# Kernel optimization log

Hardware: AMD Instinct MI355X
Metric: run time of the kernel (lower is better)

Reference implementation:

```python
import jax, jax.numpy as jnp
import numpy as np

EPS = 1e-3  # BatchNorm eps from module

def _bn(x, g, b, m, v):
    # torch BatchNorm1d (eval): (x - mean) / sqrt(var + eps) * weight + bias
    return (x - m) * (g / jnp.sqrt(v + EPS)) + b

def setup_inputs() -> dict:
    key = jax.random.key(0)
    ks = jax.random.split(key, 16)
    N, Cin, Cout, S = 1_000_000, 16, 64, 20_000
    inputs = jax.random.normal(ks[0], (N, Cin), dtype=jnp.float32)
    unq_inv = jax.random.randint(ks[1], (N,), 0, S, dtype=jnp.int32)

    def bn_params(k, c):
        k1, k2, k3, k4 = jax.random.split(k, 4)
        return (1.0 + 0.01 * jax.random.normal(k1, (c,), jnp.float32),
                0.01 * jax.random.normal(k2, (c,), jnp.float32),
                0.01 * jax.random.normal(k3, (c,), jnp.float32),
                jax.random.uniform(k4, (c,), jnp.float32, 0.5, 1.5))

    W1 = 0.1 * jax.random.normal(ks[2], (Cin, Cout), jnp.float32)
    g1, b1, m1, v1 = bn_params(ks[3], Cout)
    W2a = 0.1 * jax.random.normal(ks[4], (Cin, 2 * Cout), jnp.float32)
    g2a, b2a, m2a, v2a = bn_params(ks[5], 2 * Cout)
    W2b = 0.1 * jax.random.normal(ks[6], (2 * Cout, Cout), jnp.float32)
    g2b, b2b, m2b, v2b = bn_params(ks[7], Cout)

    return dict(inputs=inputs, unq_inv=unq_inv, num_segments=S,
                W1=W1, g1=g1, b1=b1, m1=m1, v1=v1,
                W2a=W2a, g2a=g2a, b2a=b2a, m2a=m2a, v2a=v2a,
                W2b=W2b, g2b=b2b * 0 + g2b, b2b=b2b, m2b=m2b, v2b=v2b)

def reference(inputs, unq_inv, num_segments,
              W1, g1, b1, m1, v1,
              W2a, g2a, b2a, m2a, v2a,
              W2b, g2b, b2b, m2b, v2b):
    # branch 1: Linear -> BN -> ReLU
    x = jax.nn.relu(_bn(inputs @ W1, g1, b1, m1, v1))            # [N, C]
    # branch 2: Linear -> BN -> ReLU -> Linear -> BN -> ReLU
    h = jax.nn.relu(_bn(inputs @ W2a, g2a, b2a, m2a, v2a))       # [N, 2C]
    x2 = jax.nn.relu(_bn(h @ W2b, g2b, b2b, m2b, v2b))           # [N, C]

    # segment reductions over group ids
    x_max = jax.ops.segment_max(x, unq_inv, num_segments=num_segments)  # [S, C]
    x_max = jnp.maximum(x_max, 0.0)  # empty segments -> 0 (x >= 0 post-ReLU)
    group_sum = jax.ops.segment_sum(x, unq_inv, num_segments=num_segments)  # [S, C]
    max_pool = jnp.max(x2, axis=0)                                # [C], global pool
    max_pool = jnp.broadcast_to(max_pool[None, :], x_max.shape)   # [S, C]

    feat = jnp.concatenate((group_sum, x_max, max_pool), axis=1)  # [S, 3C]
    # channel shuffle with groups=3
    S_, C3 = feat.shape
    feat = feat.reshape(S_, 3, C3 // 3).transpose(0, 2, 1).reshape(S_, C3)
    return feat
```

## Files before the change

### kernel.cpp

```cpp
#include <hip/hip_runtime.h>

#define EPS 1e-3f

#define OFF_T2B    7168
#define OFF_MPP    7232
#define OFF_MPF    11328
#define OFF_CNT    11392
#define OFF_OFFS   31408
#define OFF_CUR    51424
#define OFF_INPS   71424

typedef short short8 __attribute__((ext_vector_type(8)));
typedef float f32x4 __attribute__((ext_vector_type(4)));

union U4 { unsigned u[4]; short8 s8; uint4 u4; };

__device__ inline unsigned short f2bf(float f) {
    unsigned u = __float_as_uint(f);
    return (unsigned short)((u + 0x7FFFu + ((u >> 16) & 1u)) >> 16);
}

__global__ __launch_bounds__(256) void init_k(
    const float* __restrict__ W1,
    const float* __restrict__ g1, const float* __restrict__ b1,
    const float* __restrict__ m1, const float* __restrict__ v1,
    const float* __restrict__ W2a,
    const float* __restrict__ g2a, const float* __restrict__ b2a,
    const float* __restrict__ m2a, const float* __restrict__ v2a,
    const float* __restrict__ W2b,
    const float* __restrict__ g2b, const float* __restrict__ b2b,
    const float* __restrict__ m2b, const float* __restrict__ v2b,
    unsigned short* __restrict__ wsu, float* __restrict__ wsf,
    const int* __restrict__ unq, int* __restrict__ cnt, int N)
{
    const int t = threadIdx.x;
    if (blockIdx.x == 0) {
        for (int i = t; i < 2048; i += 256) {
            int mt = i >> 9, lane = (i >> 3) & 63, j = i & 7;
            int c = lane & 15, g = lane >> 4;
            int k = g * 8 + j, ch = mt * 16 + c;
            float s = g1[ch] * rsqrtf(v1[ch] + EPS);
            float val = (k < 16) ? W1[k * 64 + ch] * s
                      : (k == 16 ? b1[ch] - m1[ch] * s : 0.f);
            wsu[i] = f2bf(val);
        }
        for (int i = t; i < 4096; i += 256) {
            int mt = i >> 9, lane = (i >> 3) & 63, j = i & 7;
            int c = lane & 15, g = lane >> 4;
            int k = g * 8 + j, ch = mt * 16 + c;
            float s = g2a[ch] * rsqrtf(v2a[ch] + EPS);
            float val = (k < 16) ? W2a[k * 128 + ch] * s
                      : (k == 16 ? b2a[ch] - m2a[ch] * s : 0.f);
            wsu[2048 + i] = f2bf(val);
        }
        for (int i = t; i < 8192; i += 256) {
            int f = i >> 9, lane = (i >> 3) & 63, j = i & 7;
            int mt = f >> 2, ks = f & 3;
            int c = lane & 15, g = lane >> 4;
            int k = ks * 32 + g * 8 + j, ch = mt * 16 + c;
            float s = g2b[ch] * rsqrtf(v2b[ch] + EPS);
            wsu[6144 + i] = f2bf(W2b[k * 64 + ch] * s);
        }
        if (t < 64) {
            float s = g2b[t] * rsqrtf(v2b[t] + EPS);
            wsf[OFF_T2B + t] = b2b[t] - m2b[t] * s;
        }
    } else {
        const int i = (blockIdx.x - 1) * 256 + t;
        if (i < N) atomicAdd(&cnt[unq[i]], 1);
    }
}

__global__ __launch_bounds__(1024) void scan_k(
    const int* __restrict__ cnt, int* __restrict__ offs,
    int* __restrict__ cur, int S)
{
    __shared__ int tot[1024];
    const int t = threadIdx.x;
    const int E = (S + 1023) >> 10;
    const int i0 = t * E;
    int run = 0;
    for (int j = 0; j < E; ++j) {
        const int i = i0 + j;
        run += (i < S) ? cnt[i] : 0;
    }
    tot[t] = run;
    __syncthreads();
    for (int d = 1; d < 1024; d <<= 1) {
        int x = (t >= d) ? tot[t - d] : 0;
        __syncthreads();
        tot[t] += x;
        __syncthreads();
    }
    int base = (t == 0) ? 0 : tot[t - 1];
    for (int j = 0; j < E; ++j) {
        const int i = i0 + j;
        if (i < S) {
            offs[i] = base;
            cur[i]  = base;
            base += cnt[i];
        }
    }
    if (t == 1023) offs[S] = tot[1023];
}

__global__ __launch_bounds__(256, 3) void scatbr2_k(
    const float* __restrict__ inputs,
    const int*   __restrict__ unq,
    int*         __restrict__ cur,
    uint4*       __restrict__ inpS,
    const uint4* __restrict__ wsw,
    const float* __restrict__ wsf,
    float* __restrict__ mpp,
    int N)
{
    __shared__ __align__(16) char scrs[4][2][4096];
    __shared__ float mpb[64];

    const int tid  = threadIdx.x;
    const int wv   = tid >> 6;
    const int lane = tid & 63;
    const int c = lane & 15;
    const int g = lane >> 4;

    if (tid < 64) mpb[tid] = 0.f;
    __syncthreads();

    short8 w2a[8], w2b[16];
    #pragma unroll
    for (int mt = 0; mt < 8; ++mt) {
        U4 t; t.u4 = wsw[256 + mt * 64 + lane]; w2a[mt] = t.s8;
    }
    #pragma unroll
    for (int f = 0; f < 16; ++f) {
        U4 t; t.u4 = wsw[768 + f * 64 + lane]; w2b[f] = t.s8;
    }

    const long wave_pt0 = (long)blockIdx.x * 256 + (long)wv * 64;
    const long nrem_w = (long)N - wave_pt0;

    const long ip = wave_pt0 + lane;
    const bool lane_ok = (ip < (long)N) && (nrem_w > 0);
    int pos = 0;
    if (lane_ok) pos = atomicAdd(&cur[unq[ip]], 1);

    const f32x4 zero4 = {0.f, 0.f, 0.f, 0.f};
    float mp[16];
    #pragma unroll
    for (int j = 0; j < 16; ++j) mp[j] = -3.0e38f;

    #pragma unroll
    for (int ti = 0; ti < 4; ++ti) {
        if ((long)ti * 16 >= nrem_w) break;
        const bool act = (long)(ti * 16 + c) < nrem_w;
        char* scr = scrs[wv][ti & 1];

        U4 bf;
        if (g < 2) {
            const long row = act ? (wave_pt0 + ti * 16 + c) : (long)(N - 1);
            const float4* p = reinterpret_cast<const float4*>(inputs + row * 16 + g * 8);
            float4 f0 = p[0], f1 = p[1];
            asm("v_cvt_pk_bf16_f32 %0, %1, %2" : "=v"(bf.u[0]) : "v"(f0.x), "v"(f0.y));
            asm("v_cvt_pk_bf16_f32 %0, %1, %2" : "=v"(bf.u[1]) : "v"(f0.z), "v"(f0.w));
            asm("v_cvt_pk_bf16_f32 %0, %1, %2" : "=v"(bf.u[2]) : "v"(f1.x), "v"(f1.y));
            asm("v_cvt_pk_bf16_f32 %0, %1, %2" : "=v"(bf.u[3]) : "v"(f1.z), "v"(f1.w));
            if (!act) { bf.u[0] = 0u; bf.u[1] = 0u; bf.u[2] = 0u; bf.u[3] = 0u; }
        } else {
            bf.u[0] = (g == 2 && act) ? 0x00003F80u : 0u;
            bf.u[1] = 0u; bf.u[2] = 0u; bf.u[3] = 0u;
        }

        const int posc = __shfl(pos, ti * 16 + c, 64);
        if (g < 2 && act)
            inpS[(size_t)posc * 2 + g] = bf.u4;

        __builtin_amdgcn_wave_barrier();
        #pragma unroll
        for (int mt = 0; mt < 8; ++mt) {
            f32x4 hT = __builtin_amdgcn_mfma_f32_16x16x32_bf16(w2a[mt], bf.s8, zero4, 0, 0, 0);
            float h0 = fmaxf(hT[0], 0.f), h1 = fmaxf(hT[1], 0.f);
            float h2 = fmaxf(hT[2], 0.f), h3 = fmaxf(hT[3], 0.f);
            unsigned lo, hi;
            asm("v_cvt_pk_bf16_f32 %0, %1, %2" : "=v"(lo) : "v"(h0), "v"(h1));
            asm("v_cvt_pk_bf16_f32 %0, %1, %2" : "=v"(hi) : "v"(h2), "v"(h3));
            const int gw = 2 * (mt & 1) + (g >> 1);
            *reinterpret_cast<uint2*>(
                &scr[(mt >> 1) * 1024 + (gw * 16 + c) * 16 + (g & 1) * 8])
                = make_uint2(lo, hi);
        }
        __builtin_amdgcn_wave_barrier();

        f32x4 y2t[4];
        #pragma unroll
        for (int mt = 0; mt < 4; ++mt) y2t[mt] = zero4;
        #pragma unroll
        for (int ks = 0; ks < 4; ++ks) {
            short8 hb = *reinterpret_cast<const short8*>(&scr[ks * 1024 + lane * 16]);
            #pragma unroll
            for (int mt = 0; mt < 4; ++mt)
                y2t[mt] = __builtin_amdgcn_mfma_f32_16x16x32_bf16(w2b[mt * 4 + ks], hb, y2t[mt], 0, 0, 0);
        }
        #pragma unroll
        for (int mt = 0; mt < 4; ++mt) {
            #pragma unroll
            for (int r = 0; r < 4; ++r)
                mp[mt * 4 + r] = act ? fmaxf(mp[mt * 4 + r], y2t[mt][r]) : mp[mt * 4 + r];
        }
        __builtin_amdgcn_wave_barrier();
    }

    #pragma unroll
    for (int j = 0; j < 16; ++j) {
        float x = mp[j];
        x = fmaxf(x, __shfl_xor(x, 1, 64));
        x = fmaxf(x, __shfl_xor(x, 2, 64));
        x = fmaxf(x, __shfl_xor(x, 4, 64));
        x = fmaxf(x, __shfl_xor(x, 8, 64));
        mp[j] = x;
    }
    if (c == 0) {
        #pragma unroll
        for (int mt = 0; mt < 4; ++mt)
            #pragma unroll
            for (int r = 0; r < 4; ++r) {
                const int ch = mt * 16 + g * 4 + r;
                const float v = fmaxf(mp[mt * 4 + r] + wsf[OFF_T2B + ch], 0.f);
                atomicMax(reinterpret_cast<int*>(&mpb[ch]), __float_as_int(v));
            }
    }
    __syncthreads();
    if (tid < 64)
        atomicMax(reinterpret_cast<int*>(mpp + (blockIdx.x & 63) * 64 + tid),
                  __float_as_int(mpb[tid]));
}

__global__ __launch_bounds__(64) void fin_k(
    const float* __restrict__ mpp, float* __restrict__ mpf)
{
    const int t = threadIdx.x;
    float m = 0.f;
    #pragma unroll
    for (int s = 0; s < 64; ++s)
        m = fmaxf(m, mpp[s * 64 + t]);
    mpf[t] = m;
}

__global__ __launch_bounds__(256, 6) void seg1_k(
    const uint4* __restrict__ inpS,
    const int*   __restrict__ offs,
    const uint4* __restrict__ wsw,
    const float* __restrict__ mpf,
    float* __restrict__ out,
    int S)
{
    __shared__ float scr3[4][192];

    const int tid  = threadIdx.x;
    const int wv   = tid >> 6;
    const int lane = tid & 63;
    const int seg  = blockIdx.x * 4 + wv;
    if (seg >= S) return;

    const int c = lane & 15;
    const int g = lane >> 4;

    short8 w1[4];
    #pragma unroll
    for (int mt = 0; mt < 4; ++mt) {
        U4 t; t.u4 = wsw[mt * 64 + lane]; w1[mt] = t.s8;
    }
    const float mpl = mpf[lane];

    const int su    = __builtin_amdgcn_readfirstlane(seg);
    const int start = offs[su];
    const int end   = offs[su + 1];

    const f32x4 zero4 = {0.f, 0.f, 0.f, 0.f};
    f32x4 as[4], am[4];
    #pragma unroll
    for (int mt = 0; mt < 4; ++mt) { as[mt] = zero4; am[mt] = zero4; }

    for (int base = start; base < end; base += 64) {
        const int nrem = end - base;
        #pragma unroll
        for (int ti = 0; ti < 4; ++ti) {
            if (ti * 16 >= nrem) break;
            const bool act = (ti * 16 + c) < nrem;

            U4 bf;
            if (g < 2) {
                const int row = min(base + ti * 16 + c, end - 1);
                uint4 q = inpS[(size_t)row * 2 + g];
                bf.u[0] = act ? q.x : 0u;
                bf.u[1] = act ? q.y : 0u;
                bf.u[2] = act ? q.z : 0u;
                bf.u[3] = act ? q.w : 0u;
            } else {
                bf.u[0] = (g == 2 && act) ? 0x00003F80u : 0u;
                bf.u[1] = 0u; bf.u[2] = 0u; bf.u[3] = 0u;
            }
            #pragma unroll
            for (int mt = 0; mt < 4; ++mt) {
                f32x4 y1t = __builtin_amdgcn_mfma_f32_16x16x32_bf16(w1[mt], bf.s8, zero4, 0, 0, 0);
                #pragma unroll
                for (int r = 0; r < 4; ++r) {
                    float v = fmaxf(y1t[r], 0.f);
                    as[mt][r] += v;
                    am[mt][r]  = fmaxf(am[mt][r], v);
                }
            }
        }
    }

    #pragma unroll
    for (int mt = 0; mt < 4; ++mt) {
        #pragma unroll
        for (int r = 0; r < 4; ++r) {
            float xs = as[mt][r], xm = am[mt][r];
            xs += __shfl_xor(xs, 1, 64);  xm = fmaxf(xm, __shfl_xor(xm, 1, 64));
            xs += __shfl_xor(xs, 2, 64);  xm = fmaxf(xm, __shfl_xor(xm, 2, 64));
            xs += __shfl_xor(xs, 4, 64);  xm = fmaxf(xm, __shfl_xor(xm, 4, 64));
            xs += __shfl_xor(xs, 8, 64);  xm = fmaxf(xm, __shfl_xor(xm, 8, 64));
            as[mt][r] = xs; am[mt][r] = xm;
        }
    }

    float* sr = scr3[wv];
    if (c == 0) {
        #pragma unroll
        for (int mt = 0; mt < 4; ++mt)
            #pragma unroll
            for (int r = 0; r < 4; ++r) {
                const int ch = mt * 16 + g * 4 + r;
                sr[ch * 3 + 0] = as[mt][r];
                sr[ch * 3 + 1] = am[mt][r];
            }
    }
    sr[lane * 3 + 2] = mpl;
    __builtin_amdgcn_wave_barrier();
    asm volatile("s_waitcnt lgkmcnt(0)" ::: "memory");
    __builtin_amdgcn_sched_barrier(0);

    float* o = out + (size_t)seg * 192;
    #pragma unroll
    for (int p = 0; p < 3; ++p)
        o[p * 64 + lane] = sr[p * 64 + lane];
}

extern "C" void kernel_launch(void* const* d_in, const int* in_sizes, int n_in,
                              void* d_out, int out_size, void* d_ws, size_t ws_size,
                              hipStream_t stream)
{
    const float* inputs = (const float*)d_in[0];
    const int*   unq    = (const int*)d_in[1];
    const float* W1  = (const float*)d_in[3];
    const float* g1  = (const float*)d_in[4];
    const float* b1  = (const float*)d_in[5];
    const float* m1  = (const float*)d_in[6];
    const float* v1  = (const float*)d_in[7];
    const float* W2a = (const float*)d_in[8];
    const float* g2a = (const float*)d_in[9];
    const float* b2a = (const float*)d_in[10];
    const float* m2a = (const float*)d_in[11];
    const float* v2a = (const float*)d_in[12];
    const float* W2b = (const float*)d_in[13];
    const float* g2b = (const float*)d_in[14];
    const float* b2b = (const float*)d_in[15];
    const float* m2b = (const float*)d_in[16];
    const float* v2b = (const float*)d_in[17];

    float* wsf = (float*)d_ws;
    float* out = (float*)d_out;
    const int N = in_sizes[0] / 16;
    const int S = out_size / 192;

    float* mpp  = wsf + OFF_MPP;
    float* mpf  = wsf + OFF_MPF;
    int*   cnt  = (int*)(wsf + OFF_CNT);
    int*   offs = (int*)(wsf + OFF_OFFS);
    int*   cur  = (int*)(wsf + OFF_CUR);
    uint4* inpS = (uint4*)(wsf + OFF_INPS);

    hipMemsetAsync(mpp, 0, (size_t)(OFF_CNT + 20016 - OFF_MPP) * sizeof(float), stream);

    init_k<<<1 + (N + 255) / 256, 256, 0, stream>>>(
        W1, g1, b1, m1, v1, W2a, g2a, b2a, m2a, v2a, W2b, g2b, b2b, m2b, v2b,
        (unsigned short*)d_ws, wsf, unq, cnt, N);

    scan_k<<<1, 1024, 0, stream>>>(cnt, offs, cur, S);

    scatbr2_k<<<(N + 255) / 256, 256, 0, stream>>>(inputs, unq, cur, inpS,
                                                   (const uint4*)d_ws, wsf, mpp, N);

    fin_k<<<1, 64, 0, stream>>>(mpp, mpf);

    seg1_k<<<(S + 3) / 4, 256, 0, stream>>>(inpS, offs, (const uint4*)d_ws,
                                            mpf, out, S);
}
```

Measured before the change: 208.9 us.

## Split scatter from branch-2 kernel, move histogram into persistent branch-2 grid

Moves the segment-count atomics out of init_k into a persistent grid-stride branch-2 kernel, and splits the bf16 scatter into its own one-row-per-thread kernel that runs after the scan. This lets the branch-2 MLP and max-pool run before the prefix scan. The cost is an extra kernel launch and a second full read of the inputs. seg1_k also becomes a persistent 1024-block grid-stride loop with its occupancy hint lowered from 6 to 4, and asm barriers pin the branch-2 weights in registers.

```diff
diff --git a/kernel.cpp b/kernel.cpp
--- a/kernel.cpp
+++ b/kernel.cpp
@@ -30,44 +30,38 @@
     const float* __restrict__ W2b,
     const float* __restrict__ g2b, const float* __restrict__ b2b,
     const float* __restrict__ m2b, const float* __restrict__ v2b,
-    unsigned short* __restrict__ wsu, float* __restrict__ wsf,
-    const int* __restrict__ unq, int* __restrict__ cnt, int N)
+    unsigned short* __restrict__ wsu, float* __restrict__ wsf)
 {
     const int t = threadIdx.x;
-    if (blockIdx.x == 0) {
-        for (int i = t; i < 2048; i += 256) {
-            int mt = i >> 9, lane = (i >> 3) & 63, j = i & 7;
-            int c = lane & 15, g = lane >> 4;
-            int k = g * 8 + j, ch = mt * 16 + c;
-            float s = g1[ch] * rsqrtf(v1[ch] + EPS);
-            float val = (k < 16) ? W1[k * 64 + ch] * s
-                      : (k == 16 ? b1[ch] - m1[ch] * s : 0.f);
-            wsu[i] = f2bf(val);
-        }
-        for (int i = t; i < 4096; i += 256) {
-            int mt = i >> 9, lane = (i >> 3) & 63, j = i & 7;
-            int c = lane & 15, g = lane >> 4;
-            int k = g * 8 + j, ch = mt * 16 + c;
-            float s = g2a[ch] * rsqrtf(v2a[ch] + EPS);
-            float val = (k < 16) ? W2a[k * 128 + ch] * s
-                      : (k == 16 ? b2a[ch] - m2a[ch] * s : 0.f);
-            wsu[2048 + i] = f2bf(val);
-        }
-        for (int i = t; i < 8192; i += 256) {
-            int f = i >> 9, lane = (i >> 3) & 63, j = i & 7;
-            int mt = f >> 2, ks = f & 3;
-            int c = lane & 15, g = lane >> 4;
-            int k = ks * 32 + g * 8 + j, ch = mt * 16 + c;
-            float s = g2b[ch] * rsqrtf(v2b[ch] + EPS);
-            wsu[6144 + i] = f2bf(W2b[k * 64 + ch] * s);
-        }
-        if (t < 64) {
-            float s = g2b[t] * rsqrtf(v2b[t] + EPS);
-            wsf[OFF_T2B + t] = b2b[t] - m2b[t] * s;
-        }
-    } else {
-        const int i = (blockIdx.x - 1) * 256 + t;
-        if (i < N) atomicAdd(&cnt[unq[i]], 1);
+    for (int i = t; i < 2048; i += 256) {
+        int mt = i >> 9, lane = (i >> 3) & 63, j = i & 7;
+        int c = lane & 15, g = lane >> 4;
+        int k = g * 8 + j, ch = mt * 16 + c;
+        float s = g1[ch] * rsqrtf(v1[ch] + EPS);
+        float val = (k < 16) ? W1[k * 64 + ch] * s
+                  : (k == 16 ? b1[ch] - m1[ch] * s : 0.f);
+        wsu[i] = f2bf(val);
+    }
+    for (int i = t; i < 4096; i += 256) {
+        int mt = i >> 9, lane = (i >> 3) & 63, j = i & 7;
+        int c = lane & 15, g = lane >> 4;
+        int k = g * 8 + j, ch = mt * 16 + c;
+        float s = g2a[ch] * rsqrtf(v2a[ch] + EPS);
+        float val = (k < 16) ? W2a[k * 128 + ch] * s
+                  : (k == 16 ? b2a[ch] - m2a[ch] * s : 0.f);
+        wsu[2048 + i] = f2bf(val);
+    }
+    for (int i = t; i < 8192; i += 256) {
+        int f = i >> 9, lane = (i >> 3) & 63, j = i & 7;
+        int mt = f >> 2, ks = f & 3;
+        int c = lane & 15, g = lane >> 4;
+        int k = ks * 32 + g * 8 + j, ch = mt * 16 + c;
+        float s = g2b[ch] * rsqrtf(v2b[ch] + EPS);
+        wsu[6144 + i] = f2bf(W2b[k * 64 + ch] * s);
+    }
+    if (t < 64) {
+        float s = g2b[t] * rsqrtf(v2b[t] + EPS);
+        wsf[OFF_T2B + t] = b2b[t] - m2b[t] * s;
     }
 }
 
@@ -104,11 +98,10 @@
     if (t == 1023) offs[S] = tot[1023];
 }
 
-__global__ __launch_bounds__(256, 3) void scatbr2_k(
+__global__ __launch_bounds__(256, 3) void br2_k(
     const float* __restrict__ inputs,
     const int*   __restrict__ unq,
-    int*         __restrict__ cur,
-    uint4*       __restrict__ inpS,
+    int*         __restrict__ cnt,
     const uint4* __restrict__ wsw,
     const float* __restrict__ wsf,
     float* __restrict__ mpp,
@@ -128,85 +121,85 @@
 
     short8 w2a[8], w2b[16];
     #pragma unroll
-    for (int mt = 0; mt < 8; ++mt) {
-        U4 t; t.u4 = wsw[256 + mt * 64 + lane]; w2a[mt] = t.s8;
+    for (int s = 0; s < 8; ++s) {
+        U4 t; t.u4 = wsw[256 + s * 64 + lane]; w2a[s] = t.s8;
     }
     #pragma unroll
     for (int f = 0; f < 16; ++f) {
         U4 t; t.u4 = wsw[768 + f * 64 + lane]; w2b[f] = t.s8;
     }
-
-    const long wave_pt0 = (long)blockIdx.x * 256 + (long)wv * 64;
-    const long nrem_w = (long)N - wave_pt0;
-
-    const long ip = wave_pt0 + lane;
-    const bool lane_ok = (ip < (long)N) && (nrem_w > 0);
-    int pos = 0;
-    if (lane_ok) pos = atomicAdd(&cur[unq[ip]], 1);
+    #pragma unroll
+    for (int s = 0; s < 8; ++s) asm volatile("" : "+v"(w2a[s]));
+    #pragma unroll
+    for (int f = 0; f < 16; ++f) asm volatile("" : "+v"(w2b[f]));
 
     const f32x4 zero4 = {0.f, 0.f, 0.f, 0.f};
     float mp[16];
     #pragma unroll
     for (int j = 0; j < 16; ++j) mp[j] = -3.0e38f;
 
-    #pragma unroll
-    for (int ti = 0; ti < 4; ++ti) {
-        if ((long)ti * 16 >= nrem_w) break;
-        const bool act = (long)(ti * 16 + c) < nrem_w;
-        char* scr = scrs[wv][ti & 1];
-
-        U4 bf;
-        if (g < 2) {
-            const long row = act ? (wave_pt0 + ti * 16 + c) : (long)(N - 1);
-            const float4* p = reinterpret_cast<const float4*>(inputs + row * 16 + g * 8);
-            float4 f0 = p[0], f1 = p[1];
-            asm("v_cvt_pk_bf16_f32 %0, %1, %2" : "=v"(bf.u[0]) : "v"(f0.x), "v"(f0.y));
-            asm("v_cvt_pk_bf16_f32 %0, %1, %2" : "=v"(bf.u[1]) : "v"(f0.z), "v"(f0.w));
-            asm("v_cvt_pk_bf16_f32 %0, %1, %2" : "=v"(bf.u[2]) : "v"(f1.x), "v"(f1.y));
-            asm("v_cvt_pk_bf16_f32 %0, %1, %2" : "=v"(bf.u[3]) : "v"(f1.z), "v"(f1.w));
-            if (!act) { bf.u[0] = 0u; bf.u[1] = 0u; bf.u[2] = 0u; bf.u[3] = 0u; }
-        } else {
-            bf.u[0] = (g == 2 && act) ? 0x00003F80u : 0u;
-            bf.u[1] = 0u; bf.u[2] = 0u; bf.u[3] = 0u;
+    const long stride = (long)gridDim.x * 256;
+    for (long base = (long)blockIdx.x * 256 + (long)wv * 64; base < N; base += stride) {
+        const long nrem_w = (long)N - base;
+
+        if (lane < nrem_w) atomicAdd(&cnt[unq[base + lane]], 1);
+
+        #pragma unroll
+        for (int ti = 0; ti < 4; ++ti) {
+            if ((long)ti * 16 >= nrem_w) break;
+            const bool act = (long)(ti * 16 + c) < nrem_w;
+            char* scr = scrs[wv][ti & 1];
+
+            U4 bf;
+            if (g < 2) {
+                const long row = act ? (base + ti * 16 + c) : (long)(N - 1);
+                const float4* p = reinterpret_cast<const float4*>(inputs + row * 16 + g * 8);
+                float4 f0 = p[0], f1 = p[1];
+                asm("v_cvt_pk_bf16_f32 %0, %1, %2" : "=v"(bf.u[0]) : "v"(f0.x), "v"(f0.y));
+                asm("v_cvt_pk_bf16_f32 %0, %1, %2" : "=v"(bf.u[1]) : "v"(f0.z), "v"(f0.w));
+                asm("v_cvt_pk_bf16_f32 %0, %1, %2" : "=v"(bf.u[2]) : "v"(f1.x), "v"(f1.y));
+                asm("v_cvt_pk_bf16_f32 %0, %1, %2" : "=v"(bf.u[3]) : "v"(f1.z), "v"(f1.w));
+                if (!act) { bf.u[0] = 0u; bf.u[1] = 0u; bf.u[2] = 0u; bf.u[3] = 0u; }
+            } else {
+                bf.u[0] = (g == 2 && act) ? 0x00003F80u : 0u;
+                bf.u[1] = 0u; bf.u[2] = 0u; bf.u[3] = 0u;
+            }
+
+            __builtin_amdgcn_wave_barrier();
+            #pragma unroll
+            for (int mt = 0; mt < 8; ++mt) {
+                f32x4 hT = __builtin_amdgcn_mfma_f32_16x16x32_bf16(w2a[mt], bf.s8, zero4, 0, 0, 0);
+                float h0 = fmaxf(hT[0], 0.f), h1 = fmaxf(hT[1], 0.f);
+                float h2 = fmaxf(hT[2], 0.f), h3 = fmaxf(hT[3], 0.f);
+                unsigned lo, hi;
+                asm("v_cvt_pk_bf16_f32 %0, %1, %2" : "=v"(lo) : "v"(h0), "v"(h1));
+                asm("v_cvt_pk_bf16_f32 %0, %1, %2" : "=v"(hi) : "v"(h2), "v"(h3));
+                const int gw = 2 * (mt & 1) + (g >> 1);
+                *reinterpret_cast<uint2*>(
+                    &scr[(mt >> 1) * 1024 + (gw * 16 + c) * 16 + (g & 1) * 8])
+                    = make_uint2(lo, hi);
+            }
+            __builtin_amdgcn_wave_barrier();
+
+            f32x4 y2t[4];
+            #pragma unroll
+            for (int mt = 0; mt < 4; ++mt) y2t[mt] = zero4;
+            #pragma unroll
+            for (int ks = 0; ks < 4; ++ks) {
+                short8 hb = *reinterpret_cast<const short8*>(&scr[ks * 1024 + lane * 16]);
+                #pragma unroll
+                for (int mt = 0; mt < 4; ++mt)
+                    y2t[mt] = __builtin_amdgcn_mfma_f32_16x16x32_bf16(w2b[mt * 4 + ks], hb, y2t[mt], 0, 0, 0);
+            }
+            #pragma unroll
+            for (int mt = 0; mt < 4; ++mt) {
+                #pragma unroll
+                for (int r = 0; r < 4; ++r)
+                    mp[mt * 4 + r] = act ? fmaxf(mp[mt * 4 + r], y2t[mt][r])
+                                         : mp[mt * 4 + r];
+            }
+            __builtin_amdgcn_wave_barrier();
         }
-
-        const int posc = __shfl(pos, ti * 16 + c, 64);
-        if (g < 2 && act)
-            inpS[(size_t)posc * 2 + g] = bf.u4;
-
-        __builtin_amdgcn_wave_barrier();
-        #pragma unroll
-        for (int mt = 0; mt < 8; ++mt) {
-            f32x4 hT = __builtin_amdgcn_mfma_f32_16x16x32_bf16(w2a[mt], bf.s8, zero4, 0, 0, 0);
-            float h0 = fmaxf(hT[0], 0.f), h1 = fmaxf(hT[1], 0.f);
-            float h2 = fmaxf(hT[2], 0.f), h3 = fmaxf(hT[3], 0.f);
-            unsigned lo, hi;
-            asm("v_cvt_pk_bf16_f32 %0, %1, %2" : "=v"(lo) : "v"(h0), "v"(h1));
-            asm("v_cvt_pk_bf16_f32 %0, %1, %2" : "=v"(hi) : "v"(h2), "v"(h3));
-            const int gw = 2 * (mt & 1) + (g >> 1);
-            *reinterpret_cast<uint2*>(
-                &scr[(mt >> 1) * 1024 + (gw * 16 + c) * 16 + (g & 1) * 8])
-                = make_uint2(lo, hi);
-        }
-        __builtin_amdgcn_wave_barrier();
-
-        f32x4 y2t[4];
-        #pragma unroll
-        for (int mt = 0; mt < 4; ++mt) y2t[mt] = zero4;
-        #pragma unroll
-        for (int ks = 0; ks < 4; ++ks) {
-            short8 hb = *reinterpret_cast<const short8*>(&scr[ks * 1024 + lane * 16]);
-            #pragma unroll
-            for (int mt = 0; mt < 4; ++mt)
-                y2t[mt] = __builtin_amdgcn_mfma_f32_16x16x32_bf16(w2b[mt * 4 + ks], hb, y2t[mt], 0, 0, 0);
-        }
-        #pragma unroll
-        for (int mt = 0; mt < 4; ++mt) {
-            #pragma unroll
-            for (int r = 0; r < 4; ++r)
-                mp[mt * 4 + r] = act ? fmaxf(mp[mt * 4 + r], y2t[mt][r]) : mp[mt * 4 + r];
-        }
-        __builtin_amdgcn_wave_barrier();
     }
 
     #pragma unroll
@@ -234,6 +227,34 @@
                   __float_as_int(mpb[tid]));
 }
 
+__global__ __launch_bounds__(256) void scat_k(
+    const float* __restrict__ inputs,
+    const int*   __restrict__ unq,
+    int*         __restrict__ cur,
+    uint4*       __restrict__ inpS,
+    int N)
+{
+    const int i = blockIdx.x * 256 + threadIdx.x;
+    if (i >= N) return;
+    const int seg = unq[i];
+    const int pos = atomicAdd(&cur[seg], 1);
+
+    const float4* p = reinterpret_cast<const float4*>(inputs + (size_t)i * 16);
+    float4 a0 = p[0], a1 = p[1], a2 = p[2], a3 = p[3];
+    unsigned pk[8];
+    asm("v_cvt_pk_bf16_f32 %0, %1, %2" : "=v"(pk[0]) : "v"(a0.x), "v"(a0.y));
+    asm("v_cvt_pk_bf16_f32 %0, %1, %2" : "=v"(pk[1]) : "v"(a0.z), "v"(a0.w));
+    asm("v_cvt_pk_bf16_f32 %0, %1, %2" : "=v"(pk[2]) : "v"(a1.x), "v"(a1.y));
+    asm("v_cvt_pk_bf16_f32 %0, %1, %2" : "=v"(pk[3]) : "v"(a1.z), "v"(a1.w));
+    asm("v_cvt_pk_bf16_f32 %0, %1, %2" : "=v"(pk[4]) : "v"(a2.x), "v"(a2.y));
+    asm("v_cvt_pk_bf16_f32 %0, %1, %2" : "=v"(pk[5]) : "v"(a2.z), "v"(a2.w));
+    asm("v_cvt_pk_bf16_f32 %0, %1, %2" : "=v"(pk[6]) : "v"(a3.x), "v"(a3.y));
+    asm("v_cvt_pk_bf16_f32 %0, %1, %2" : "=v"(pk[7]) : "v"(a3.z), "v"(a3.w));
+
+    inpS[(size_t)pos * 2]     = make_uint4(pk[0], pk[1], pk[2], pk[3]);
+    inpS[(size_t)pos * 2 + 1] = make_uint4(pk[4], pk[5], pk[6], pk[7]);
+}
+
 __global__ __launch_bounds__(64) void fin_k(
     const float* __restrict__ mpp, float* __restrict__ mpf)
 {
@@ -245,7 +266,7 @@
     mpf[t] = m;
 }
 
-__global__ __launch_bounds__(256, 6) void seg1_k(
+__global__ __launch_bounds__(256, 4) void seg1_k(
     const uint4* __restrict__ inpS,
     const int*   __restrict__ offs,
     const uint4* __restrict__ wsw,
@@ -258,9 +279,6 @@
     const int tid  = threadIdx.x;
     const int wv   = tid >> 6;
     const int lane = tid & 63;
-    const int seg  = blockIdx.x * 4 + wv;
-    if (seg >= S) return;
-
     const int c = lane & 15;
     const int g = lane >> 4;
 
@@ -270,81 +288,85 @@
         U4 t; t.u4 = wsw[mt * 64 + lane]; w1[mt] = t.s8;
     }
     const float mpl = mpf[lane];
-
-    const int su    = __builtin_amdgcn_readfirstlane(seg);
-    const int start = offs[su];
-    const int end   = offs[su + 1];
-
+    float* sr = scr3[wv];
     const f32x4 zero4 = {0.f, 0.f, 0.f, 0.f};
-    f32x4 as[4], am[4];
-    #pragma unroll
-    for (int mt = 0; mt < 4; ++mt) { as[mt] = zero4; am[mt] = zero4; }
-
-    for (int base = start; base < end; base += 64) {
-        const int nrem = end - base;
+
+    const int nw = gridDim.x * 4;
+    for (int seg = blockIdx.x * 4 + wv; seg < S; seg += nw) {
+        const int su    = __builtin_amdgcn_readfirstlane(seg);
+        const int start = offs[su];
+        const int end   = offs[su + 1];
+
+        f32x4 as[4], am[4];
         #pragma unroll
-        for (int ti = 0; ti < 4; ++ti) {
-            if (ti * 16 >= nrem) break;
-            const bool act = (ti * 16 + c) < nrem;
-
-            U4 bf;
-            if (g < 2) {
-                const int row = min(base + ti * 16 + c, end - 1);
-                uint4 q = inpS[(size_t)row * 2 + g];
-                bf.u[0] = act ? q.x : 0u;
-                bf.u[1] = act ? q.y : 0u;
-                bf.u[2] = act ? q.z : 0u;
-                bf.u[3] = act ? q.w : 0u;
-            } else {
-                bf.u[0] = (g == 2 && act) ? 0x00003F80u : 0u;
-                bf.u[1] = 0u; bf.u[2] = 0u; bf.u[3] = 0u;
-            }
-            #pragma unroll
-            for (int mt = 0; mt < 4; ++mt) {
-                f32x4 y1t = __builtin_amdgcn_mfma_f32_16x16x32_bf16(w1[mt], bf.s8, zero4, 0, 0, 0);
+        for (int mt = 0; mt < 4; ++mt) { as[mt] = zero4; am[mt] = zero4; }
+
+        for (int base = start; base < end; base += 64) {
+            const int nrem = end - base;
+            #pragma unroll
+            for (int ti = 0; ti < 4; ++ti) {
+                if (ti * 16 >= nrem) break;
+                const bool act = (ti * 16 + c) < nrem;
+
+                U4 bf;
+                if (g < 2) {
+                    const int row = min(base + ti * 16 + c, end - 1);
+                    uint4 q = inpS[(size_t)row * 2 + g];
+                    bf.u[0] = act ? q.x : 0u;
+                    bf.u[1] = act ? q.y : 0u;
+                    bf.u[2] = act ? q.z : 0u;
+                    bf.u[3] = act ? q.w : 0u;
+                } else {
+                    bf.u[0] = (g == 2 && act) ? 0x00003F80u : 0u;
+                    bf.u[1] = 0u; bf.u[2] = 0u; bf.u[3] = 0u;
+                }
+                #pragma unroll
+                for (int mt = 0; mt < 4; ++mt) {
+                    f32x4 y1t = __builtin_amdgcn_mfma_f32_16x16x32_bf16(w1[mt], bf.s8, zero4, 0, 0, 0);
+                    #pragma unroll
+                    for (int r = 0; r < 4; ++r) {
+                        float v = fmaxf(y1t[r], 0.f);
+                        as[mt][r] += v;
+                        am[mt][r]  = fmaxf(am[mt][r], v);
+                    }
+                }
+            }
+        }
+
+        #pragma unroll
+        for (int mt = 0; mt < 4; ++mt) {
+            #pragma unroll
+            for (int r = 0; r < 4; ++r) {
+                float xs = as[mt][r], xm = am[mt][r];
+                xs += __shfl_xor(xs, 1, 64);  xm = fmaxf(xm, __shfl_xor(xm, 1, 64));
+                xs += __shfl_xor(xs, 2, 64);  xm = fmaxf(xm, __shfl_xor(xm, 2, 64));
+                xs += __shfl_xor(xs, 4, 64);  xm = fmaxf(xm, __shfl_xor(xm, 4, 64));
+                xs += __shfl_xor(xs, 8, 64);  xm = fmaxf(xm, __shfl_xor(xm, 8, 64));
+                as[mt][r] = xs; am[mt][r] = xm;
+            }
+        }
+
+        if (c == 0) {
+            #pragma unroll
+            for (int mt = 0; mt < 4; ++mt)
                 #pragma unroll
                 for (int r = 0; r < 4; ++r) {
-                    float v = fmaxf(y1t[r], 0.f);
-                    as[mt][r] += v;
-                    am[mt][r]  = fmaxf(am[mt][r], v);
+                    const int ch = mt * 16 + g * 4 + r;
+                    sr[ch * 3 + 0] = as[mt][r];
+                    sr[ch * 3 + 1] = am[mt][r];
                 }
-            }
         }
-    }
-
-    #pragma unroll
-    for (int mt = 0; mt < 4; ++mt) {
+        sr[lane * 3 + 2] = mpl;
+        __builtin_amdgcn_wave_barrier();
+        asm volatile("s_waitcnt lgkmcnt(0)" ::: "memory");
+        __builtin_amdgcn_sched_barrier(0);
+
+        float* o = out + (size_t)seg * 192;
         #pragma unroll
-        for (int r = 0; r < 4; ++r) {
-            float xs = as[mt][r], xm = am[mt][r];
-            xs += __shfl_xor(xs, 1, 64);  xm = fmaxf(xm, __shfl_xor(xm, 1, 64));
-            xs += __shfl_xor(xs, 2, 64);  xm = fmaxf(xm, __shfl_xor(xm, 2, 64));
-            xs += __shfl_xor(xs, 4, 64);  xm = fmaxf(xm, __shfl_xor(xm, 4, 64));
-            xs += __shfl_xor(xs, 8, 64);  xm = fmaxf(xm, __shfl_xor(xm, 8, 64));
-            as[mt][r] = xs; am[mt][r] = xm;
-        }
-    }
-
-    float* sr = scr3[wv];
-    if (c == 0) {
-        #pragma unroll
-        for (int mt = 0; mt < 4; ++mt)
-            #pragma unroll
-            for (int r = 0; r < 4; ++r) {
-                const int ch = mt * 16 + g * 4 + r;
-                sr[ch * 3 + 0] = as[mt][r];
-                sr[ch * 3 + 1] = am[mt][r];
-            }
-    }
-    sr[lane * 3 + 2] = mpl;
-    __builtin_amdgcn_wave_barrier();
-    asm volatile("s_waitcnt lgkmcnt(0)" ::: "memory");
-    __builtin_amdgcn_sched_barrier(0);
-
-    float* o = out + (size_t)seg * 192;
-    #pragma unroll
-    for (int p = 0; p < 3; ++p)
-        o[p * 64 + lane] = sr[p * 64 + lane];
+        for (int p = 0; p < 3; ++p)
+            o[p * 64 + lane] = sr[p * 64 + lane];
+        __builtin_amdgcn_wave_barrier();
+    }
 }
 
 extern "C" void kernel_launch(void* const* d_in, const int* in_sizes, int n_in,
@@ -383,17 +405,20 @@
 
     hipMemsetAsync(mpp, 0, (size_t)(OFF_CNT + 20016 - OFF_MPP) * sizeof(float), stream);
 
-    init_k<<<1 + (N + 255) / 256, 256, 0, stream>>>(
-        W1, g1, b1, m1, v1, W2a, g2a, b2a, m2a, v2a, W2b, g2b, b2b, m2b, v2b,
-        (unsigned short*)d_ws, wsf, unq, cnt, N);
+    init_k<<<1, 256, 0, stream>>>(W1, g1, b1, m1, v1,
+                                  W2a, g2a, b2a, m2a, v2a,
+                                  W2b, g2b, b2b, m2b, v2b,
+                                  (unsigned short*)d_ws, wsf);
+
+    br2_k<<<1024, 256, 0, stream>>>(inputs, unq, cnt, (const uint4*)d_ws, wsf,
+                                    mpp, N);
 
     scan_k<<<1, 1024, 0, stream>>>(cnt, offs, cur, S);
 
-    scatbr2_k<<<(N + 255) / 256, 256, 0, stream>>>(inputs, unq, cur, inpS,
-                                                   (const uint4*)d_ws, wsf, mpp, N);
+    scat_k<<<(N + 255) / 256, 256, 0, stream>>>(inputs, unq, cur, inpS, N);
 
     fin_k<<<1, 64, 0, stream>>>(mpp, mpf);
 
-    seg1_k<<<(S + 3) / 4, 256, 0, stream>>>(inpS, offs, (const uint4*)d_ws,
-                                            mpf, out, S);
-}
+    seg1_k<<<1024, 256, 0, stream>>>(inpS, offs, (const uint4*)d_ws,
+                                     mpf, out, S);
+}
```

Result: slower. 222.5 us (+6.5%).
